# Kernel optimization log

Measured on AMD Instinct MI355X. Metric: run time of the kernel, lower is better.

Reference implementation:

```python
import jax, jax.numpy as jnp
import numpy as np

B, C, H, W = 4, 2048, 48, 48
HC = 256

def setup_inputs() -> dict:
    key = jax.random.key(0)
    k1, k2, k3, k4 = jax.random.split(key, 4)
    scale = 1.0 / np.sqrt(C)
    return {
        "left_features": jax.random.normal(k1, (B, C, H, W), dtype=jnp.float32),
        "right_features": jax.random.normal(k2, (B, C, H, W), dtype=jnp.float32),
        "Wq": jax.random.normal(k3, (HC, C), dtype=jnp.float32) * scale,
        "bq": jnp.zeros((HC,), dtype=jnp.float32),
        "Wk": jax.random.normal(k4, (HC, C), dtype=jnp.float32) * scale,
        "bk": jnp.zeros((HC,), dtype=jnp.float32),
    }

def _coattn(query_feat, ref_feat, Wq, bq, Wk, bk):
    b, c, h, w = query_feat.shape
    hw = h * w
    # 1x1 convs == per-pixel channel projections
    Q = jnp.einsum('bchw,oc->bohw', query_feat, Wq) + bq[None, :, None, None]
    K = jnp.einsum('bchw,oc->bohw', ref_feat, Wk) + bk[None, :, None, None]
    Qf = Q.reshape(b, -1, hw)          # [b, hc, hw_q]
    Kf = K.reshape(b, -1, hw)          # [b, hc, hw_k]
    V = ref_feat.reshape(b, c, hw)     # [b, c, hw_k]
    # attention scores over all spatial pairs, softmax over reference positions
    attn = jax.nn.softmax(jnp.einsum('bci,bcj->bij', Qf, Kf), axis=-1)  # [b, hw_q, hw_k]
    out = jnp.einsum('bij,bcj->bci', attn, V)  # [b, c, hw_q]
    return out.reshape(b, c, h, w)

def reference(left_features, right_features, Wq, bq, Wk, bk):
    weighted_r = _coattn(left_features, right_features, Wq, bq, Wk, bk)
    weighted_l = _coattn(right_features, left_features, Wq, bq, Wk, bk)
    # rearrange '[orig, weighted] two b c h w -> b (two c) h w' == channel concat
    left_attended = jnp.concatenate([left_features, weighted_l], axis=1)
    right_attended = jnp.concatenate([right_features, weighted_r], axis=1)
    return (left_attended, right_attended)
```

## Files before the change

kernel.cpp:

```cpp
#include <hip/hip_runtime.h>
#include <stdint.h>


#define NB 4
#define NC 2048
#define NHW 2304
#define NHC 256
#define NT 36

typedef _Float16 f16;
typedef __attribute__((ext_vector_type(4))) _Float16 f16x4;
typedef __attribute__((ext_vector_type(8))) _Float16 f16x8;
typedef __attribute__((ext_vector_type(4))) float f32x4;

static __device__ __forceinline__ void glds16(const void* g, void* lds) {
  __builtin_amdgcn_global_load_lds(
      (const __attribute__((address_space(1))) uint32_t*)g,
      (__attribute__((address_space(3))) uint32_t*)lds, 16, 0, 0);
}

__global__ __launch_bounds__(256) void k_prep(
    const float* __restrict__ xl, const float* __restrict__ xr,
    float* __restrict__ out, f16* __restrict__ Xh, f16* __restrict__ Xt) {
  const int z = blockIdx.z, side = z >> 2, b = z & 3;
  const float* X = (side ? xr : xl) + (size_t)b * NC * NHW;
  const int hw0 = blockIdx.x * 64, c0 = blockIdx.y * 64;
  const int t = threadIdx.x;
  const int colb = (t & 15) * 4;
  const int r0 = t >> 4;
  __shared__ f16 Lt[64 * 64];
  float* outb = out + (size_t)side * ((size_t)NB * 2 * NC * NHW) + (size_t)b * (2 * NC * NHW);
  f16* Xhb = Xh + (size_t)side * ((size_t)NB * NC * NHW) + (size_t)b * NC * NHW;
  f16* Xtb = Xt + (size_t)side * ((size_t)NB * NHW * NC) + (size_t)b * NHW * NC;
#pragma unroll
  for (int p = 0; p < 4; ++p) {
    int r = r0 + p * 16;
    size_t go = (size_t)(c0 + r) * NHW + hw0 + colb;
    float4 v = *(const float4*)&X[go];
    *(float4*)&outb[go] = v;
    f16x4 h; h[0] = (f16)v.x; h[1] = (f16)v.y; h[2] = (f16)v.z; h[3] = (f16)v.w;
    *(f16x4*)&Xhb[go] = h;
#pragma unroll
    for (int j = 0; j < 4; ++j) {
      int row = colb + j;
      int byte = row * 128 + ((r * 2) ^ ((((row >> 2) & 7)) << 4));
      *(f16*)((char*)Lt + byte) = h[j];
    }
  }
  __syncthreads();
#pragma unroll
  for (int p = 0; p < 2; ++p) {
    int idx = p * 256 + t;
    int row = idx >> 3, ch = idx & 7;
    int byte = row * 128 + (((ch ^ ((row >> 2) & 7))) << 4);
    f16x8 vv = *(const f16x8*)((char*)Lt + byte);
    *(f16x8*)&Xtb[(size_t)(hw0 + row) * NC + c0 + ch * 8] = vv;
  }
}

__global__ __launch_bounds__(256) void k_w16(
    const float* __restrict__ wq, const float* __restrict__ wk, f16* __restrict__ Ws) {
  const int N4 = NHC * NC / 4;
  int idx = blockIdx.x * 256 + threadIdx.x;
  const float* src = (idx < N4) ? wq : wk;
  int e4 = (idx < N4) ? idx : idx - N4;
  float4 v = ((const float4*)src)[e4];
  f16x4 h; h[0] = (f16)v.x; h[1] = (f16)v.y; h[2] = (f16)v.z; h[3] = (f16)v.w;
  ((f16x4*)Ws)[idx] = h;
}

__global__ __launch_bounds__(256) void k_proj(
    const f16* __restrict__ Ws, const f16* __restrict__ Xt0,
    const float* __restrict__ bq, const float* __restrict__ bk,
    f16* __restrict__ Yt0) {
  __shared__ f16 LA[2][128 * 32], LB[2][128 * 32];
  const int side = blockIdx.z;
  const f16* Xt = Xt0 + (size_t)side * ((size_t)NB * NHW * NC);
  f16* Yt = Yt0 + (size_t)side * ((size_t)NB * NHW * 512);
  const int n0 = blockIdx.x * 128;
  const int m0 = blockIdx.y * 128;
  const int tid = threadIdx.x, wv = tid >> 6, ln = tid & 63;
  const int lr = ln & 15, lh = ln >> 4;
  const int wm = wv >> 1, wn = wv & 1;
  f32x4 acc[4][4];
#pragma unroll
  for (int mi = 0; mi < 4; ++mi)
#pragma unroll
    for (int ni = 0; ni < 4; ++ni)
#pragma unroll
      for (int q = 0; q < 4; ++q) acc[mi][ni][q] = 0.f;

  auto stage = [&](int bi, int ks) {
    int k0 = ks * 32;
#pragma unroll
    for (int rep = 0; rep < 2; ++rep) {
      int u = rep * 256 + wv * 64 + ln;
      int r = u >> 2, k8 = (u & 3) * 8;
      int ub8 = (rep * 256 + wv * 64) * 8;
      glds16(Ws + (size_t)(m0 + r) * NC + k0 + k8, &LA[bi][ub8]);
      glds16(Xt + (size_t)(n0 + r) * NC + k0 + k8, &LB[bi][ub8]);
    }
  };
  auto compute = [&](int bi) {
    f16x8 af[4], bf[4];
#pragma unroll
    for (int mi = 0; mi < 4; ++mi)
      af[mi] = *(const f16x8*)&LA[bi][(wm * 64 + mi * 16 + lr) * 32 + lh * 8];
#pragma unroll
    for (int ni = 0; ni < 4; ++ni)
      bf[ni] = *(const f16x8*)&LB[bi][(wn * 64 + ni * 16 + lr) * 32 + lh * 8];
#pragma unroll
    for (int mi = 0; mi < 4; ++mi)
#pragma unroll
      for (int ni = 0; ni < 4; ++ni)
        acc[mi][ni] = __builtin_amdgcn_mfma_f32_16x16x32_f16(af[mi], bf[ni], acc[mi][ni], 0, 0, 0);
  };

  stage(0, 0);
  __syncthreads();
  int cur = 0;
  for (int ks = 0; ks < 63; ++ks) {
    stage(cur ^ 1, ks + 1);
    compute(cur);
    __syncthreads();
    cur ^= 1;
  }
  compute(cur);

#pragma unroll
  for (int mi = 0; mi < 4; ++mi)
#pragma unroll
    for (int ni = 0; ni < 4; ++ni) {
      int ob = m0 + wm * 64 + mi * 16 + lh * 4;
      int i = n0 + wn * 64 + ni * 16 + lr;
      f16x4 hv;
#pragma unroll
      for (int q = 0; q < 4; ++q) {
        int o = ob + q;
        float bias = (o < NHC) ? bq[o] : bk[o - NHC];
        hv[q] = (f16)(acc[mi][ni][q] + bias);
      }
      *(f16x4*)&Yt[(size_t)i * 512 + ob] = hv;
    }
}

__global__ __launch_bounds__(256) void k_scores(
    const f16* __restrict__ Yt, float* __restrict__ S0, float* __restrict__ S1,
    int dir0) {
  __shared__ f16 LA[2][128 * 32], LB[2][128 * 32];
  const size_t YTS = (size_t)NB * NHW * 512;
  const int z = blockIdx.z;
  const int dir = dir0 + (z >> 2);
  const int b = z & 3;
  const int i0 = blockIdx.x * 128, j0 = blockIdx.y * 128;
  const int tid = threadIdx.x, wv = tid >> 6, ln = tid & 63;
  const int lr = ln & 15, lh = ln >> 4;
  const int wm = wv >> 1, wn = wv & 1;
  const f16* Qb = Yt + (size_t)dir * YTS + (size_t)b * NHW * 512;
  const f16* Kb = Yt + (size_t)(1 - dir) * YTS + NHC + (size_t)b * NHW * 512;
  f32x4 acc[4][4];
#pragma unroll
  for (int mi = 0; mi < 4; ++mi)
#pragma unroll
    for (int ni = 0; ni < 4; ++ni)
#pragma unroll
      for (int q = 0; q < 4; ++q) acc[mi][ni][q] = 0.f;

  auto stage = [&](int bi, int ks) {
    int k0 = ks * 32;
#pragma unroll
    for (int rep = 0; rep < 2; ++rep) {
      int u = rep * 256 + wv * 64 + ln;
      int r = u >> 2, k8 = (u & 3) * 8;
      int ub8 = (rep * 256 + wv * 64) * 8;
      glds16(Qb + (size_t)(i0 + r) * 512 + k0 + k8, &LA[bi][ub8]);
      glds16(Kb + (size_t)(j0 + r) * 512 + k0 + k8, &LB[bi][ub8]);
    }
  };
  auto compute = [&](int bi) {
    f16x8 af[4], bf[4];
#pragma unroll
    for (int mi = 0; mi < 4; ++mi)
      af[mi] = *(const f16x8*)&LA[bi][(wm * 64 + mi * 16 + lr) * 32 + lh * 8];
#pragma unroll
    for (int ni = 0; ni < 4; ++ni)
      bf[ni] = *(const f16x8*)&LB[bi][(wn * 64 + ni * 16 + lr) * 32 + lh * 8];
#pragma unroll
    for (int mi = 0; mi < 4; ++mi)
#pragma unroll
      for (int ni = 0; ni < 4; ++ni)
        acc[mi][ni] = __builtin_amdgcn_mfma_f32_16x16x32_f16(af[mi], bf[ni], acc[mi][ni], 0, 0, 0);
  };

  stage(0, 0);
  __syncthreads();
  int cur = 0;
  for (int ks = 0; ks < 7; ++ks) {
    stage(cur ^ 1, ks + 1);
    compute(cur);
    __syncthreads();
    cur ^= 1;
  }
  compute(cur);

  float* Sb = (dir ? S1 : S0) + (size_t)b * NHW * NHW;
#pragma unroll
  for (int mi = 0; mi < 4; ++mi)
#pragma unroll
    for (int ni = 0; ni < 4; ++ni) {
      int i = i0 + wm * 64 + mi * 16 + lh * 4;
      int j = j0 + wn * 64 + ni * 16 + lr;
#pragma unroll
      for (int q = 0; q < 4; ++q)
        Sb[(size_t)(i + q) * NHW + j] = acc[mi][ni][q];
    }
}

__global__ __launch_bounds__(256) void k_softmax(
    float* __restrict__ S0, float* __restrict__ S1) {
  const int rid = blockIdx.x;
  const int ROWS = NB * NHW;
  float* rp = (rid < ROWS ? S0 : S1) + (size_t)(rid < ROWS ? rid : rid - ROWS) * NHW;
  const int t = threadIdx.x;
  float v[9];
  float m = -3.4e38f;
#pragma unroll
  for (int k = 0; k < 9; ++k) { v[k] = rp[t + 256 * k]; m = fmaxf(m, v[k]); }
#pragma unroll
  for (int off = 32; off > 0; off >>= 1) m = fmaxf(m, __shfl_xor(m, off));
  __shared__ float red[4];
  __shared__ float red2[4];
  const int wv = t >> 6, ln = t & 63;
  if (ln == 0) red[wv] = m;
  __syncthreads();
  m = fmaxf(fmaxf(red[0], red[1]), fmaxf(red[2], red[3]));
  float s = 0.f;
#pragma unroll
  for (int k = 0; k < 9; ++k) { v[k] = expf(v[k] - m); s += v[k]; }
#pragma unroll
  for (int off = 32; off > 0; off >>= 1) s += __shfl_xor(s, off);
  if (ln == 0) red2[wv] = s;
  __syncthreads();
  float inv = 1.0f / (red2[0] + red2[1] + red2[2] + red2[3]);
  f16* op = (f16*)rp;
#pragma unroll
  for (int k = 0; k < 9; ++k) op[t + 256 * k] = (f16)(v[k] * inv);
}

__global__ __launch_bounds__(512, 2) void k_pv8(
    const f16* __restrict__ V0, const f16* __restrict__ V1,
    const float* __restrict__ S0, const float* __restrict__ S1,
    float* __restrict__ out, int ndirs, long long ob0, long long ob1) {
  extern __shared__ __align__(16) f16 SH[];

  const int nwg = ndirs * 288;
  const int bid = blockIdx.x;
  const int wg = (bid & 7) * (nwg >> 3) + (bid >> 3);
  const int n = wg % 9;
  const int r1 = wg / 9;
  const int m = r1 & 7;
  const int r2 = r1 >> 3;
  const int b = r2 & 3;
  const int dir = r2 >> 2;

  const f16* Vb = (dir ? V1 : V0) + (size_t)b * NC * NHW;
  const char* Sb = (const char*)(dir ? S1 : S0) + (size_t)b * NHW * NHW * 4;
  const long long obase = dir ? ob1 : ob0;
  const int c0 = m * 256, i0 = n * 256;
  const int tid = threadIdx.x, wv = tid >> 6, ln = tid & 63;
  const int lr = ln & 15, lg = ln >> 4;
  const int wm = wv >> 2, wn = wv & 3;

  const int fr = tid >> 3;
  const int scolb = ((tid & 7) * 16) ^ ((fr & 7) << 4);
  const f16* aSrc = Vb + (size_t)(c0 + fr) * NHW + (scolb >> 1);
  const char* bSrc = Sb + (size_t)(i0 + fr) * 9216 + scolb;
  const int ldsW = wv * 512;

  auto stA = [&](int bf, int t2, int r) {
    glds16(aSrc + (size_t)r * 64 * NHW + (size_t)t2 * 64,
           SH + bf * 16384 + r * 4096 + ldsW);
  };
  auto stB = [&](int bf, int t2, int r) {
    glds16(bSrc + (size_t)r * 64 * 9216 + t2 * 128,
           SH + 32768 + bf * 16384 + r * 4096 + ldsW);
  };
  auto rdA = [&](int bf, int mi, int ks) -> f16x8 {
    int row = wm * 128 + mi * 16 + lr;
    int colb = (ks * 64 + lg * 16) ^ ((row & 7) << 4);
    return *(const f16x8*)((const char*)(SH + bf * 16384) + row * 128 + colb);
  };
  auto rdB = [&](int bf, int ni, int ks) -> f16x8 {
    int row = wn * 64 + ni * 16 + lr;
    int colb = (ks * 64 + lg * 16) ^ ((row & 7) << 4);
    return *(const f16x8*)((const char*)(SH + 32768 + bf * 16384) + row * 128 + colb);
  };

  f32x4 acc[8][4];
#pragma unroll
  for (int mi = 0; mi < 8; ++mi)
#pragma unroll
    for (int ni = 0; ni < 4; ++ni)
#pragma unroll
      for (int q = 0; q < 4; ++q) acc[mi][ni][q] = 0.f;

  f16x8 Af[4][2], Bn0[2][2], Bn1[2][2];

#pragma unroll
  for (int r = 0; r < 4; ++r) stA(0, 0, r);
#pragma unroll
  for (int r = 0; r < 4; ++r) stB(0, 0, r);
#pragma unroll
  for (int r = 0; r < 4; ++r) stA(1, 1, r);
#pragma unroll
  for (int r = 0; r < 4; ++r) stB(1, 1, r);
  asm volatile("s_waitcnt vmcnt(8)" ::: "memory");
  asm volatile("s_barrier" ::: "memory");

  for (int t = 0; t < NT; ++t) {
    const int cb = t & 1;
    const bool s2 = (t + 2 < NT);
#pragma unroll
    for (int mi = 0; mi < 4; ++mi) { Af[mi][0] = rdA(cb, mi, 0); Af[mi][1] = rdA(cb, mi, 1); }
#pragma unroll
    for (int ni = 0; ni < 2; ++ni) { Bn0[ni][0] = rdB(cb, ni, 0); Bn0[ni][1] = rdB(cb, ni, 1); }
    asm volatile("s_barrier" ::: "memory");
    asm volatile("s_waitcnt lgkmcnt(0)" ::: "memory");
    __builtin_amdgcn_sched_barrier(0);
    __builtin_amdgcn_s_setprio(1);
#pragma unroll
    for (int ks = 0; ks < 2; ++ks)
#pragma unroll
      for (int mi = 0; mi < 4; ++mi)
#pragma unroll
        for (int ni = 0; ni < 2; ++ni)
          acc[mi][ni] = __builtin_amdgcn_mfma_f32_16x16x32_f16(Af[mi][ks], Bn0[ni][ks], acc[mi][ni], 0, 0, 0);
    __builtin_amdgcn_s_setprio(0);
    asm volatile("s_barrier" ::: "memory");
#pragma unroll
    for (int ni = 0; ni < 2; ++ni) { Bn1[ni][0] = rdB(cb, 2 + ni, 0); Bn1[ni][1] = rdB(cb, 2 + ni, 1); }
    if (s2) { stA(cb, t + 2, 0); stA(cb, t + 2, 2); }
    asm volatile("s_barrier" ::: "memory");
    asm volatile("s_waitcnt lgkmcnt(0)" ::: "memory");
    __builtin_amdgcn_sched_barrier(0);
    __builtin_amdgcn_s_setprio(1);
#pragma unroll
    for (int ks = 0; ks < 2; ++ks)
#pragma unroll
      for (int mi = 0; mi < 4; ++mi)
#pragma unroll
        for (int ni = 0; ni < 2; ++ni)
          acc[mi][2 + ni] = __builtin_amdgcn_mfma_f32_16x16x32_f16(Af[mi][ks], Bn1[ni][ks], acc[mi][2 + ni], 0, 0, 0);
    __builtin_amdgcn_s_setprio(0);
    asm volatile("s_barrier" ::: "memory");
#pragma unroll
    for (int mi = 0; mi < 4; ++mi) { Af[mi][0] = rdA(cb, 4 + mi, 0); Af[mi][1] = rdA(cb, 4 + mi, 1); }
    if (s2) { stB(cb, t + 2, 0); stB(cb, t + 2, 1); }
    asm volatile("s_barrier" ::: "memory");
    asm volatile("s_waitcnt lgkmcnt(0)" ::: "memory");
    __builtin_amdgcn_sched_barrier(0);
    __builtin_amdgcn_s_setprio(1);
#pragma unroll
    for (int ks = 0; ks < 2; ++ks)
#pragma unroll
      for (int mi = 0; mi < 4; ++mi)
#pragma unroll
        for (int ni = 0; ni < 2; ++ni)
          acc[4 + mi][2 + ni] = __builtin_amdgcn_mfma_f32_16x16x32_f16(Af[mi][ks], Bn1[ni][ks], acc[4 + mi][2 + ni], 0, 0, 0);
    __builtin_amdgcn_s_setprio(0);
    asm volatile("s_barrier" ::: "memory");
    if (s2) { stA(cb, t + 2, 1); stA(cb, t + 2, 3); stB(cb, t + 2, 2); stB(cb, t + 2, 3); }
    __builtin_amdgcn_s_setprio(1);
#pragma unroll
    for (int ks = 0; ks < 2; ++ks)
#pragma unroll
      for (int mi = 0; mi < 4; ++mi)
#pragma unroll
        for (int ni = 0; ni < 2; ++ni)
          acc[4 + mi][ni] = __builtin_amdgcn_mfma_f32_16x16x32_f16(Af[mi][ks], Bn0[ni][ks], acc[4 + mi][ni], 0, 0, 0);
    __builtin_amdgcn_s_setprio(0);
    if (s2)                { asm volatile("s_waitcnt vmcnt(8)" ::: "memory"); }
    else if (t + 1 < NT)   { asm volatile("s_waitcnt vmcnt(0)" ::: "memory"); }
    asm volatile("s_barrier" ::: "memory");
  }

  float* ob = out + obase + (size_t)b * (2 * NC * NHW);
#pragma unroll
  for (int mi = 0; mi < 8; ++mi)
#pragma unroll
    for (int ni = 0; ni < 4; ++ni) {
      int c = c0 + wm * 128 + mi * 16 + lg * 4;
      int i = i0 + wn * 64 + ni * 16 + lr;
#pragma unroll
      for (int q = 0; q < 4; ++q)
        ob[(size_t)(NC + c + q) * NHW + i] = acc[mi][ni][q];
    }
}

extern "C" void kernel_launch(void* const* d_in, const int* in_sizes, int n_in,
                              void* d_out, int out_size, void* d_ws, size_t ws_size,
                              hipStream_t stream) {
  const float* xl = (const float*)d_in[0];
  const float* xr = (const float*)d_in[1];
  const float* wq = (const float*)d_in[2];
  const float* bq = (const float*)d_in[3];
  const float* wk = (const float*)d_in[4];
  const float* bk = (const float*)d_in[5];
  float* out = (float*)d_out;
  char* ws = (char*)d_ws;

  const size_t XH_BYTES = (size_t)2 * NB * NC * NHW * 2;
  const size_t WS_BYTES = (size_t)512 * NC * 2;
  const size_t YT_BYTES = (size_t)2 * NB * NHW * 512 * 2;
  const size_t S_BYTES  = (size_t)NB * NHW * NHW * 4;

  f16* Xh = (f16*)ws;
  f16* Ws_ = (f16*)(ws + XH_BYTES);
  f16* Yt = (f16*)(ws + XH_BYTES + WS_BYTES);
  char* rest = ws + XH_BYTES + WS_BYTES + YT_BYTES;

  const size_t xh_side = (size_t)NB * NC * NHW;
  const long long obA = (long long)NB * 2 * NC * NHW;
  const long long obB = 0;

  const bool merged = ws_size >= XH_BYTES + WS_BYTES + YT_BYTES + 2 * S_BYTES;

  if (merged) {
    float* S0 = (float*)rest;
    char* rest2 = rest + S_BYTES;
    f16* Xt = (f16*)rest2;
    float* S1 = (float*)rest2;

    k_prep<<<dim3(36, 32, 8), dim3(256), 0, stream>>>(xl, xr, out, Xh, Xt);
    k_w16<<<dim3(1024), dim3(256), 0, stream>>>(wq, wk, Ws_);
    k_proj<<<dim3(72, 4, 2), dim3(256), 0, stream>>>(Ws_, Xt, bq, bk, Yt);

    k_scores<<<dim3(18, 18, 8), dim3(256), 0, stream>>>(Yt, S0, S1, 0);
    k_softmax<<<dim3(2 * NB * NHW), dim3(256), 0, stream>>>(S0, S1);
    k_pv8<<<dim3(576), dim3(512), 131072, stream>>>(
        Xh + xh_side, Xh, S0, S1, out, 2, obA, obB);
  } else {
    f16* Xt = (f16*)rest;
    float* S = (float*)rest;

    k_prep<<<dim3(36, 32, 8), dim3(256), 0, stream>>>(xl, xr, out, Xh, Xt);
    k_w16<<<dim3(1024), dim3(256), 0, stream>>>(wq, wk, Ws_);
    k_proj<<<dim3(72, 4, 2), dim3(256), 0, stream>>>(Ws_, Xt, bq, bk, Yt);

    k_scores<<<dim3(18, 18, 4), dim3(256), 0, stream>>>(Yt, S, S, 0);
    k_softmax<<<dim3(NB * NHW), dim3(256), 0, stream>>>(S, S);
    k_pv8<<<dim3(288), dim3(512), 131072, stream>>>(
        Xh + xh_side, Xh + xh_side, S, S, out, 1, obA, obA);

    k_scores<<<dim3(18, 18, 4), dim3(256), 0, stream>>>(Yt, S, S, 1);
    k_softmax<<<dim3(NB * NHW), dim3(256), 0, stream>>>(S, S);
    k_pv8<<<dim3(288), dim3(512), 131072, stream>>>(
        Xh, Xh, S, S, out, 1, obB, obB);
  }
}
```

Before: 439.2 us.

## Load PV B operand directly from global into registers with triple-buffered A in LDS

```diff
diff --git a/kernel.cpp b/kernel.cpp
--- a/kernel.cpp
+++ b/kernel.cpp
@@ -274,26 +274,20 @@
   const int fr = tid >> 3;
   const int scolb = ((tid & 7) * 16) ^ ((fr & 7) << 4);
   const f16* aSrc = Vb + (size_t)(c0 + fr) * NHW + (scolb >> 1);
-  const char* bSrc = Sb + (size_t)(i0 + fr) * 9216 + scolb;
   const int ldsW = wv * 512;
 
-  auto stA = [&](int bf, int t2, int r) {
+  auto stA = [&](int slot, int t2, int r) {
     glds16(aSrc + (size_t)r * 64 * NHW + (size_t)t2 * 64,
-           SH + bf * 16384 + r * 4096 + ldsW);
-  };
-  auto stB = [&](int bf, int t2, int r) {
-    glds16(bSrc + (size_t)r * 64 * 9216 + t2 * 128,
-           SH + 32768 + bf * 16384 + r * 4096 + ldsW);
-  };
-  auto rdA = [&](int bf, int mi, int ks) -> f16x8 {
+           SH + slot * 16384 + r * 4096 + ldsW);
+  };
+  auto rdA = [&](int slot, int mi, int ks) -> f16x8 {
     int row = wm * 128 + mi * 16 + lr;
     int colb = (ks * 64 + lg * 16) ^ ((row & 7) << 4);
-    return *(const f16x8*)((const char*)(SH + bf * 16384) + row * 128 + colb);
-  };
-  auto rdB = [&](int bf, int ni, int ks) -> f16x8 {
-    int row = wn * 64 + ni * 16 + lr;
-    int colb = (ks * 64 + lg * 16) ^ ((row & 7) << 4);
-    return *(const f16x8*)((const char*)(SH + 32768 + bf * 16384) + row * 128 + colb);
+    return *(const f16x8*)((const char*)(SH + slot * 16384) + row * 128 + colb);
+  };
+  const char* bR = Sb + (size_t)(i0 + wn * 64 + lr) * 9216 + lg * 16;
+  auto ldB = [&](int t2, int ni, int ks) -> f16x8 {
+    return *(const f16x8*)(bR + (size_t)ni * (16 * 9216) + t2 * 128 + ks * 64);
   };
 
   f32x4 acc[8][4];
@@ -304,84 +298,67 @@
 #pragma unroll
       for (int q = 0; q < 4; ++q) acc[mi][ni][q] = 0.f;
 
-  f16x8 Af[4][2], Bn0[2][2], Bn1[2][2];
+  f16x8 BA[4][2], BB[4][2];
 
 #pragma unroll
   for (int r = 0; r < 4; ++r) stA(0, 0, r);
 #pragma unroll
-  for (int r = 0; r < 4; ++r) stB(0, 0, r);
-#pragma unroll
   for (int r = 0; r < 4; ++r) stA(1, 1, r);
 #pragma unroll
-  for (int r = 0; r < 4; ++r) stB(1, 1, r);
-  asm volatile("s_waitcnt vmcnt(8)" ::: "memory");
+  for (int ni = 0; ni < 4; ++ni) {
+    BA[ni][0] = ldB(0, ni, 0);
+    BA[ni][1] = ldB(0, ni, 1);
+  }
+  asm volatile("s_waitcnt vmcnt(12)" ::: "memory");
   asm volatile("s_barrier" ::: "memory");
-
-  for (int t = 0; t < NT; ++t) {
-    const int cb = t & 1;
-    const bool s2 = (t + 2 < NT);
-#pragma unroll
-    for (int mi = 0; mi < 4; ++mi) { Af[mi][0] = rdA(cb, mi, 0); Af[mi][1] = rdA(cb, mi, 1); }
-#pragma unroll
-    for (int ni = 0; ni < 2; ++ni) { Bn0[ni][0] = rdB(cb, ni, 0); Bn0[ni][1] = rdB(cb, ni, 1); }
+  __builtin_amdgcn_sched_barrier(0);
+
+  auto tile = [&](int t, f16x8 (&Bc)[4][2], f16x8 (&Bn)[4][2]) {
+    const int slot = t % 3;
+    f16x8 Af[4][2];
+#pragma unroll
+    for (int mi = 0; mi < 4; ++mi) { Af[mi][0] = rdA(slot, mi, 0); Af[mi][1] = rdA(slot, mi, 1); }
+    if (t + 1 < NT) {
+#pragma unroll
+      for (int ni = 0; ni < 4; ++ni) {
+        Bn[ni][0] = ldB(t + 1, ni, 0);
+        Bn[ni][1] = ldB(t + 1, ni, 1);
+      }
+    }
+    __builtin_amdgcn_s_setprio(1);
+#pragma unroll
+    for (int ks = 0; ks < 2; ++ks)
+#pragma unroll
+      for (int mi = 0; mi < 4; ++mi)
+#pragma unroll
+        for (int ni = 0; ni < 4; ++ni)
+          acc[mi][ni] = __builtin_amdgcn_mfma_f32_16x16x32_f16(Af[mi][ks], Bc[ni][ks], acc[mi][ni], 0, 0, 0);
+    __builtin_amdgcn_s_setprio(0);
+#pragma unroll
+    for (int mi = 0; mi < 4; ++mi) { Af[mi][0] = rdA(slot, 4 + mi, 0); Af[mi][1] = rdA(slot, 4 + mi, 1); }
+    if (t + 2 < NT) {
+      int s2 = (t + 2) % 3;
+#pragma unroll
+      for (int r = 0; r < 4; ++r) stA(s2, t + 2, r);
+    }
+    __builtin_amdgcn_s_setprio(1);
+#pragma unroll
+    for (int ks = 0; ks < 2; ++ks)
+#pragma unroll
+      for (int mi = 0; mi < 4; ++mi)
+#pragma unroll
+        for (int ni = 0; ni < 4; ++ni)
+          acc[4 + mi][ni] = __builtin_amdgcn_mfma_f32_16x16x32_f16(Af[mi][ks], Bc[ni][ks], acc[4 + mi][ni], 0, 0, 0);
+    __builtin_amdgcn_s_setprio(0);
+    if (t + 2 < NT)      { asm volatile("s_waitcnt vmcnt(12)" ::: "memory"); }
+    else if (t + 1 < NT) { asm volatile("s_waitcnt vmcnt(8)" ::: "memory"); }
     asm volatile("s_barrier" ::: "memory");
-    asm volatile("s_waitcnt lgkmcnt(0)" ::: "memory");
     __builtin_amdgcn_sched_barrier(0);
-    __builtin_amdgcn_s_setprio(1);
-#pragma unroll
-    for (int ks = 0; ks < 2; ++ks)
-#pragma unroll
-      for (int mi = 0; mi < 4; ++mi)
-#pragma unroll
-        for (int ni = 0; ni < 2; ++ni)
-          acc[mi][ni] = __builtin_amdgcn_mfma_f32_16x16x32_f16(Af[mi][ks], Bn0[ni][ks], acc[mi][ni], 0, 0, 0);
-    __builtin_amdgcn_s_setprio(0);
-    asm volatile("s_barrier" ::: "memory");
-#pragma unroll
-    for (int ni = 0; ni < 2; ++ni) { Bn1[ni][0] = rdB(cb, 2 + ni, 0); Bn1[ni][1] = rdB(cb, 2 + ni, 1); }
-    if (s2) { stA(cb, t + 2, 0); stA(cb, t + 2, 2); }
-    asm volatile("s_barrier" ::: "memory");
-    asm volatile("s_waitcnt lgkmcnt(0)" ::: "memory");
-    __builtin_amdgcn_sched_barrier(0);
-    __builtin_amdgcn_s_setprio(1);
-#pragma unroll
-    for (int ks = 0; ks < 2; ++ks)
-#pragma unroll
-      for (int mi = 0; mi < 4; ++mi)
-#pragma unroll
-        for (int ni = 0; ni < 2; ++ni)
-          acc[mi][2 + ni] = __builtin_amdgcn_mfma_f32_16x16x32_f16(Af[mi][ks], Bn1[ni][ks], acc[mi][2 + ni], 0, 0, 0);
-    __builtin_amdgcn_s_setprio(0);
-    asm volatile("s_barrier" ::: "memory");
-#pragma unroll
-    for (int mi = 0; mi < 4; ++mi) { Af[mi][0] = rdA(cb, 4 + mi, 0); Af[mi][1] = rdA(cb, 4 + mi, 1); }
-    if (s2) { stB(cb, t + 2, 0); stB(cb, t + 2, 1); }
-    asm volatile("s_barrier" ::: "memory");
-    asm volatile("s_waitcnt lgkmcnt(0)" ::: "memory");
-    __builtin_amdgcn_sched_barrier(0);
-    __builtin_amdgcn_s_setprio(1);
-#pragma unroll
-    for (int ks = 0; ks < 2; ++ks)
-#pragma unroll
-      for (int mi = 0; mi < 4; ++mi)
-#pragma unroll
-        for (int ni = 0; ni < 2; ++ni)
-          acc[4 + mi][2 + ni] = __builtin_amdgcn_mfma_f32_16x16x32_f16(Af[mi][ks], Bn1[ni][ks], acc[4 + mi][2 + ni], 0, 0, 0);
-    __builtin_amdgcn_s_setprio(0);
-    asm volatile("s_barrier" ::: "memory");
-    if (s2) { stA(cb, t + 2, 1); stA(cb, t + 2, 3); stB(cb, t + 2, 2); stB(cb, t + 2, 3); }
-    __builtin_amdgcn_s_setprio(1);
-#pragma unroll
-    for (int ks = 0; ks < 2; ++ks)
-#pragma unroll
-      for (int mi = 0; mi < 4; ++mi)
-#pragma unroll
-        for (int ni = 0; ni < 2; ++ni)
-          acc[4 + mi][ni] = __builtin_amdgcn_mfma_f32_16x16x32_f16(Af[mi][ks], Bn0[ni][ks], acc[4 + mi][ni], 0, 0, 0);
-    __builtin_amdgcn_s_setprio(0);
-    if (s2)                { asm volatile("s_waitcnt vmcnt(8)" ::: "memory"); }
-    else if (t + 1 < NT)   { asm volatile("s_waitcnt vmcnt(0)" ::: "memory"); }
-    asm volatile("s_barrier" ::: "memory");
+  };
+
+  for (int t = 0; t < NT; t += 2) {
+    tile(t, BA, BB);
+    tile(t + 1, BB, BA);
   }
 
   float* ob = out + obase + (size_t)b * (2 * NC * NHW);
@@ -437,7 +414,7 @@
 
     k_scores<<<dim3(18, 18, 8), dim3(256), 0, stream>>>(Yt, S0, S1, 0);
     k_softmax<<<dim3(2 * NB * NHW), dim3(256), 0, stream>>>(S0, S1);
-    k_pv8<<<dim3(576), dim3(512), 131072, stream>>>(
+    k_pv8<<<dim3(576), dim3(512), 98304, stream>>>(
         Xh + xh_side, Xh, S0, S1, out, 2, obA, obB);
   } else {
     f16* Xt = (f16*)rest;
@@ -449,12 +426,12 @@
 
     k_scores<<<dim3(18, 18, 4), dim3(256), 0, stream>>>(Yt, S, S, 0);
     k_softmax<<<dim3(NB * NHW), dim3(256), 0, stream>>>(S, S);
-    k_pv8<<<dim3(288), dim3(512), 131072, stream>>>(
+    k_pv8<<<dim3(288), dim3(512), 98304, stream>>>(
         Xh + xh_side, Xh + xh_side, S, S, out, 1, obA, obA);
 
     k_scores<<<dim3(18, 18, 4), dim3(256), 0, stream>>>(Yt, S, S, 1);
     k_softmax<<<dim3(NB * NHW), dim3(256), 0, stream>>>(S, S);
-    k_pv8<<<dim3(288), dim3(512), 131072, stream>>>(
+    k_pv8<<<dim3(288), dim3(512), 98304, stream>>>(
         Xh, Xh, S, S, out, 1, obB, obB);
   }
 }
```

After: 561.6 us. 1.28x slower.
